# Kernel tuning notes

Measured on AMD Instinct MI355X. Metric: run time of the kernel, lower is better.

The kernel has to match this reference:

```python
import jax, jax.numpy as jnp
import numpy as np

L = 2048      # sequence length (self.len)
DIM = 1024    # model dim
DPOS = 128    # positional encoding dim
B = 4
EPS = 1e-5


def make_pe(length, d):
    # standard sinusoidal positional encoding, shape [length, d]
    pos = np.arange(length)[:, None].astype(np.float32)
    div = np.exp(-np.arange(0, d, 2).astype(np.float32) * (np.log(10000.0) / d))
    pe = np.zeros((length, d), dtype=np.float32)
    pe[:, 0::2] = np.sin(pos * div)
    pe[:, 1::2] = np.cos(pos * div)
    return jnp.asarray(pe)


def setup_inputs() -> dict:
    key = jax.random.key(0)
    ks = jax.random.split(key, 16)
    s = lambda fan_in: 1.0 / np.sqrt(fan_in)
    inp = {
        "z": jax.random.normal(ks[0], (B, L, DIM), jnp.float32),
        "x": jax.random.normal(ks[1], (B, L, DIM), jnp.float32),
        "a": jax.random.normal(ks[2], (1,), jnp.float32),
        "pe": make_pe(L, DPOS),
        # torch Linear weights stored [out, in]
        "w_pos1": jax.random.normal(ks[3], (DPOS + DIM, DPOS), jnp.float32) * s(DPOS),
        "b_pos1": jnp.zeros((DPOS + DIM,), jnp.float32),
        "w_pos2": jax.random.normal(ks[4], (DIM, DPOS + DIM), jnp.float32) * s(DPOS + DIM),
        "b_pos2": jnp.zeros((DIM,), jnp.float32),
        "w1": jax.random.normal(ks[5], (DIM * 2, DIM), jnp.float32) * s(DIM),
        "b1": jnp.zeros((DIM * 2,), jnp.float32),
        "w2": jax.random.normal(ks[6], (DIM, DIM * 2), jnp.float32) * s(DIM * 2),
        "b2": jnp.zeros((DIM,), jnp.float32),
        "w3": jax.random.normal(ks[7], (DIM * 2, DIM), jnp.float32) * s(DIM),
        "b3": jnp.zeros((DIM * 2,), jnp.float32),
        "w4": jax.random.normal(ks[8], (DIM, DIM * 2), jnp.float32) * s(DIM * 2),
        "b4": jnp.zeros((DIM,), jnp.float32),
        "ln_g": jnp.ones((DIM,), jnp.float32),
        "ln_b": jnp.zeros((DIM,), jnp.float32),
    }
    return inp


def _layer_norm(v, g, b):
    mu = jnp.mean(v, axis=-1, keepdims=True)
    var = jnp.var(v, axis=-1, keepdims=True)
    return (v - mu) * jax.lax.rsqrt(var + EPS) * g + b


def _lin(v, w, b):
    return v @ w.T + b


def reference(z, x, a, pe, w_pos1, b_pos1, w_pos2, b_pos2,
              w1, b1, w2, b2, w3, b3, w4, b4, ln_g, ln_b):
    zn = _layer_norm(z, ln_g, ln_b)                       # [B, L, D]
    fz = jnp.fft.rfft(zn, n=2 * L, axis=1)                # [B, L+1, D] complex
    expa = jnp.exp(a)                                     # [1]
    window = jnp.exp(-jnp.arange(L, dtype=jnp.float32) * expa)  # [L]
    h = _lin(pe, w_pos1, b_pos1)                          # [L, DPOS+D]
    h = jax.nn.gelu(h, approximate=False)
    h = _lin(h, w_pos2, b_pos2)                           # [L, D] (dropout eval = id)
    wfh = jnp.fft.rfft(window[:, None] * h, n=2 * L, axis=0)  # [L+1, D]
    cwhz = jnp.fft.irfft(wfh * fz, axis=1)[:, :L, :]      # [B, L, D]
    x1 = _lin(x, w1, b1)
    x1 = jax.nn.gelu(x1, approximate=False)
    x1 = _lin(x1, w2, b2)
    x1 = x1 * cwhz + z
    y = _layer_norm(x1, ln_g, ln_b)
    y = _lin(y, w3, b3)
    y = jax.nn.gelu(y, approximate=False)
    y = _lin(y, w4, b4)
    return y + x1
```

## Files before the change

### kernel.cpp

```cpp
#include <hip/hip_runtime.h>
#include <hip/hip_bf16.h>
#include <cmath>

typedef __hip_bfloat16 bf16;
typedef __attribute__((ext_vector_type(8))) short bf16x8;
typedef __attribute__((ext_vector_type(4))) float f32x4;

static __device__ __forceinline__ float b2f(bf16 v) { return __bfloat162float(v); }
static __device__ __forceinline__ bf16 f2b(float v) { return __float2bfloat16(v); }
static __device__ __forceinline__ float us2f(unsigned short u) {
  return __uint_as_float(((unsigned)u) << 16);
}

static __device__ __forceinline__ void gl2lds16(const bf16* g, bf16* l) {
  __builtin_amdgcn_global_load_lds(
      (const __attribute__((address_space(1))) void*)g,
      (__attribute__((address_space(3))) void*)l, 16, 0, 0);
}

static __device__ __forceinline__ float gelu_fast(float v) {
  float u = v * (0.7978845608f + 0.0356774081f * v * v);
  float e = __expf(2.f * u);
  return v * (e * __frcp_rn(e + 1.f));
}

struct CvtSegs { const float* src[7]; int blk_off[8]; };
__global__ __launch_bounds__(256) void cvt7_k(CvtSegs s, bf16* __restrict__ dst0)
{
  int b = blockIdx.x;
  int seg = 0;
#pragma unroll
  for (int i = 0; i < 6; ++i) seg += (b >= s.blk_off[i + 1]) ? 1 : 0;
  const float* src = s.src[seg] + (size_t)(b - s.blk_off[seg]) * 1024;
  bf16* dst = dst0 + (size_t)b * 1024;
  int idx = threadIdx.x * 4;
  float4 v = *(const float4*)(src + idx);
  union { bf16 bb[4]; ushort4 u; } o;
  o.bb[0] = f2b(v.x); o.bb[1] = f2b(v.y); o.bb[2] = f2b(v.z); o.bb[3] = f2b(v.w);
  *(ushort4*)(dst + idx) = o.u;
}

__global__ __launch_bounds__(256) void cvt_k(const float* __restrict__ in,
                                             bf16* __restrict__ out, int n)
{
  int idx = (blockIdx.x * 256 + threadIdx.x) * 4;
  if (idx >= n) return;
  float4 v = *(const float4*)(in + idx);
  union { bf16 b[4]; ushort4 u; } o;
  o.b[0] = f2b(v.x); o.b[1] = f2b(v.y); o.b[2] = f2b(v.z); o.b[3] = f2b(v.w);
  *(ushort4*)(out + idx) = o.u;
}

__global__ __launch_bounds__(256) void ln_k(const float* __restrict__ X, bf16* __restrict__ Y,
                                            const float* __restrict__ gamma,
                                            const float* __restrict__ beta)
{
  __shared__ float red[16];
  const int row = blockIdx.x, tid = threadIdx.x;
  float4 v = *(const float4*)(X + (size_t)row * 1024 + tid * 4);
  float s  = v.x + v.y + v.z + v.w;
  float s2 = v.x * v.x + v.y * v.y + v.z * v.z + v.w * v.w;
#pragma unroll
  for (int m = 32; m; m >>= 1) { s += __shfl_xor(s, m, 64); s2 += __shfl_xor(s2, m, 64); }
  const int wid = tid >> 6;
  if ((tid & 63) == 0) { red[wid] = s; red[wid + 8] = s2; }
  __syncthreads();
  s  = red[0] + red[1] + red[2] + red[3];
  s2 = red[8] + red[9] + red[10] + red[11];
  const float mu  = s * (1.f / 1024.f);
  const float var = s2 * (1.f / 1024.f) - mu * mu;
  const float rs  = rsqrtf(var + 1e-5f);
  float4 g = *(const float4*)(gamma + tid * 4);
  float4 bt = *(const float4*)(beta + tid * 4);
  union { bf16 b[4]; ushort4 u; } o;
  o.b[0] = f2b((v.x - mu) * rs * g.x + bt.x);
  o.b[1] = f2b((v.y - mu) * rs * g.y + bt.y);
  o.b[2] = f2b((v.z - mu) * rs * g.z + bt.z);
  o.b[3] = f2b((v.w - mu) * rs * g.w + bt.w);
  *(ushort4*)(Y + (size_t)row * 1024 + tid * 4) = o.u;
}

template<int EPI>
__global__ __launch_bounds__(256, 3) void gemm_k(
    const bf16* __restrict__ A, const bf16* __restrict__ W,
    const float* __restrict__ bias, void* __restrict__ Out,
    const void* __restrict__ aux0, const void* __restrict__ aux1,
    int M, int N, int K)
{
  __shared__ bf16 As[3][128 * 32];
  __shared__ bf16 Bs[3][128 * 32];
  const int tid = threadIdx.x;
  const int wid = tid >> 6, lane = tid & 63;
  const int quad = lane >> 4, l16 = lane & 15;
  const int wm = wid >> 1, wn = wid & 1;
  const int m0 = blockIdx.y * 128, n0 = blockIdx.x * 128;

  f32x4 acc[4][4];
#pragma unroll
  for (int i = 0; i < 4; ++i)
#pragma unroll
    for (int j = 0; j < 4; ++j) acc[i][j] = (f32x4){0.f, 0.f, 0.f, 0.f};

  const bf16 *ga[2], *gb[2];
  int ldso[2];
#pragma unroll
  for (int r = 0; r < 2; ++r) {
    int p = r * 256 + wid * 64 + lane;
    int row = p >> 2;
    int sko = ((p & 3) ^ ((p >> 3) & 3)) << 3;
    ga[r] = A + (size_t)(m0 + row) * K + sko;
    gb[r] = W + (size_t)(n0 + row) * K + sko;
    ldso[r] = (r * 256 + wid * 64) * 8;
  }
  int apos[4], bpos[4];
#pragma unroll
  for (int i = 0; i < 4; ++i) {
    int ar = wm * 64 + i * 16 + l16;
    apos[i] = (ar * 4 + (quad ^ ((ar >> 1) & 3))) * 8;
    int br = wn * 64 + i * 16 + l16;
    bpos[i] = (br * 4 + (quad ^ ((br >> 1) & 3))) * 8;
  }

  const int niter = K >> 5;
#pragma unroll
  for (int t = 0; t < 2; ++t)
#pragma unroll
    for (int r = 0; r < 2; ++r) {
      gl2lds16(ga[r] + t * 32, &As[t][ldso[r]]);
      gl2lds16(gb[r] + t * 32, &Bs[t][ldso[r]]);
    }

  int cur = 0;
  for (int k = 0; k < niter; ++k) {
    if (k == niter - 1) { asm volatile("s_waitcnt vmcnt(0)" ::: "memory"); }
    else               { asm volatile("s_waitcnt vmcnt(4)" ::: "memory"); }
    asm volatile("s_barrier" ::: "memory");

    const bf16* as = As[cur];
    const bf16* bs = Bs[cur];
    bf16x8 af[4], bfr[4];
#pragma unroll
    for (int i = 0; i < 4; ++i) af[i]  = *(const bf16x8*)(as + apos[i]);
#pragma unroll
    for (int j = 0; j < 4; ++j) bfr[j] = *(const bf16x8*)(bs + bpos[j]);
    asm volatile("s_waitcnt lgkmcnt(0)" ::: "memory");

    if (k + 2 < niter) {
      int nb = cur + 2; if (nb >= 3) nb -= 3;
#pragma unroll
      for (int r = 0; r < 2; ++r) {
        gl2lds16(ga[r] + (k + 2) * 32, &As[nb][ldso[r]]);
        gl2lds16(gb[r] + (k + 2) * 32, &Bs[nb][ldso[r]]);
      }
    }
#pragma unroll
    for (int i = 0; i < 4; ++i)
#pragma unroll
      for (int j = 0; j < 4; ++j)
        acc[i][j] = __builtin_amdgcn_mfma_f32_16x16x32_bf16(af[i], bfr[j], acc[i][j], 0, 0, 0);
    cur += 1; if (cur == 3) cur = 0;
  }

  float expa = 0.f;
  if (EPI == 1) expa = expf(((const float*)aux0)[0]);
#pragma unroll
  for (int i = 0; i < 4; ++i) {
    const int gm_base = m0 + wm * 64 + i * 16 + quad * 4;
#pragma unroll
    for (int j = 0; j < 4; ++j) {
      const int gn = n0 + wn * 64 + j * 16 + l16;
      const float bv = bias[gn];
#pragma unroll
      for (int r = 0; r < 4; ++r) {
        const int gm = gm_base + r;
        const size_t off = (size_t)gm * N + gn;
        float v = acc[i][j][r] + bv;
        if (EPI == 0) ((bf16*)Out)[off] = f2b(gelu_fast(v));
        else if (EPI == 1) ((float*)Out)[off] = v * expf(-(float)gm * expa);
        else if (EPI == 2) ((float*)Out)[off] = v * ((const float*)aux0)[off] + ((const float*)aux1)[off];
        else ((float*)Out)[off] = v + ((const float*)aux0)[off];
      }
    }
  }
}

template<int EPI>
__global__ __launch_bounds__(256, 2) void gemm256_k(
    const bf16* __restrict__ A, const bf16* __restrict__ W,
    const float* __restrict__ bias, void* __restrict__ Out,
    const void* __restrict__ aux0, const void* __restrict__ aux1,
    int M, int N, int K)
{
  __shared__ bf16 As[3][128 * 32];
  __shared__ bf16 Bs[3][256 * 32];
  const int tid = threadIdx.x;
  const int wid = tid >> 6, lane = tid & 63;
  const int quad = lane >> 4, l16 = lane & 15;
  const int wm = wid >> 1, wn = wid & 1;
  const int m0 = blockIdx.y * 128, n0 = blockIdx.x * 256;

  f32x4 acc[4][8];
#pragma unroll
  for (int i = 0; i < 4; ++i)
#pragma unroll
    for (int j = 0; j < 8; ++j) acc[i][j] = (f32x4){0.f, 0.f, 0.f, 0.f};

  const bf16 *ga[2], *gb[4];
  int ldsoA[2], ldsoB[4];
#pragma unroll
  for (int r = 0; r < 2; ++r) {
    int p = r * 256 + tid;
    int row = p >> 2;
    int sko = ((p & 3) ^ ((p >> 3) & 3)) << 3;
    ga[r] = A + (size_t)(m0 + row) * K + sko;
    ldsoA[r] = (r * 256 + wid * 64) * 8;
  }
#pragma unroll
  for (int r = 0; r < 4; ++r) {
    int p = r * 256 + tid;
    int row = p >> 2;
    int sko = ((p & 3) ^ ((p >> 3) & 3)) << 3;
    gb[r] = W + (size_t)(n0 + row) * K + sko;
    ldsoB[r] = (r * 256 + wid * 64) * 8;
  }
  int apos[4], bpos[8];
#pragma unroll
  for (int i = 0; i < 4; ++i) {
    int ar = wm * 64 + i * 16 + l16;
    apos[i] = (ar * 4 + (quad ^ ((ar >> 1) & 3))) * 8;
  }
#pragma unroll
  for (int j = 0; j < 8; ++j) {
    int br = wn * 128 + j * 16 + l16;
    bpos[j] = (br * 4 + (quad ^ ((br >> 1) & 3))) * 8;
  }

  const int niter = K >> 5;
#pragma unroll
  for (int t = 0; t < 2; ++t) {
#pragma unroll
    for (int r = 0; r < 2; ++r) gl2lds16(ga[r] + t * 32, &As[t][ldsoA[r]]);
#pragma unroll
    for (int r = 0; r < 4; ++r) gl2lds16(gb[r] + t * 32, &Bs[t][ldsoB[r]]);
  }

  int cur = 0;
  for (int k = 0; k < niter; ++k) {
    if (k == niter - 1) { asm volatile("s_waitcnt vmcnt(0)" ::: "memory"); }
    else               { asm volatile("s_waitcnt vmcnt(6)" ::: "memory"); }
    asm volatile("s_barrier" ::: "memory");

    const bf16* as = As[cur];
    const bf16* bs = Bs[cur];
    bf16x8 af[4], bfr[8];
#pragma unroll
    for (int i = 0; i < 4; ++i) af[i]  = *(const bf16x8*)(as + apos[i]);
#pragma unroll
    for (int j = 0; j < 8; ++j) bfr[j] = *(const bf16x8*)(bs + bpos[j]);
    asm volatile("s_waitcnt lgkmcnt(0)" ::: "memory");

    if (k + 2 < niter) {
      int nb = cur + 2; if (nb >= 3) nb -= 3;
#pragma unroll
      for (int r = 0; r < 2; ++r) gl2lds16(ga[r] + (k + 2) * 32, &As[nb][ldsoA[r]]);
#pragma unroll
      for (int r = 0; r < 4; ++r) gl2lds16(gb[r] + (k + 2) * 32, &Bs[nb][ldsoB[r]]);
    }
#pragma unroll
    for (int i = 0; i < 4; ++i)
#pragma unroll
      for (int j = 0; j < 8; ++j)
        acc[i][j] = __builtin_amdgcn_mfma_f32_16x16x32_bf16(af[i], bfr[j], acc[i][j], 0, 0, 0);
    cur += 1; if (cur == 3) cur = 0;
  }

#pragma unroll
  for (int i = 0; i < 4; ++i) {
    const int gm_base = m0 + wm * 64 + i * 16 + quad * 4;
#pragma unroll
    for (int j = 0; j < 8; ++j) {
      const int gn = n0 + wn * 128 + j * 16 + l16;
      const float bv = bias[gn];
#pragma unroll
      for (int r = 0; r < 4; ++r) {
        const int gm = gm_base + r;
        const size_t off = (size_t)gm * N + gn;
        float v = acc[i][j][r] + bv;
        if (EPI == 0) ((bf16*)Out)[off] = f2b(gelu_fast(v));
        else if (EPI == 2) ((float*)Out)[off] = v * ((const float*)aux0)[off] + ((const float*)aux1)[off];
        else ((float*)Out)[off] = v + ((const float*)aux0)[off];
      }
    }
  }
}

__global__ __launch_bounds__(256) void conv_k(
    const bf16* __restrict__ zn,
    const float* __restrict__ wh,
    const float* __restrict__ a,
    float* __restrict__ out)
{
  __shared__ float whs[64 * 64];
  __shared__ float znt[128 * 64];
  const int tid = threadIdx.x;
  const int dd = tid & 63, ttg = tid >> 6;
  const int t0 = blockIdx.x * 64, d0 = blockIdx.y * 64, b = blockIdx.z;
  const float expa = expf(a[0]);
  const float smax = 20.7f / expa;
  const unsigned short* znu = (const unsigned short*)zn;

  float acc[16];
#pragma unroll
  for (int q = 0; q < 16; ++q) acc[q] = 0.f;

  for (int sb = 0; sb <= t0 + 63; sb += 64) {
    if ((float)sb > smax) break;
    float4 wv4[4];
#pragma unroll
    for (int i = 0; i < 4; ++i) {
      int cc = tid + 256 * i;
      int row = cc >> 4, dq = (cc & 15) * 4;
      wv4[i] = *(const float4*)&wh[(size_t)(sb + row) * 1024 + d0 + dq];
    }
    ushort4 zv4[8];
#pragma unroll
    for (int i = 0; i < 8; ++i) {
      int cc = tid + 256 * i;
      int row = cc >> 4, dq = (cc & 15) * 4;
      int u = t0 - sb - 64 + row;
      zv4[i] = (u >= 0) ? *(const ushort4*)&znu[((size_t)b * 2048 + u) * 1024 + d0 + dq]
                        : make_ushort4(0, 0, 0, 0);
    }
#pragma unroll
    for (int i = 0; i < 4; ++i) {
      int cc = tid + 256 * i;
      *(float4*)&whs[(cc >> 4) * 64 + (cc & 15) * 4] = wv4[i];
    }
#pragma unroll
    for (int i = 0; i < 8; ++i) {
      int cc = tid + 256 * i;
      float4 o;
      o.x = us2f(zv4[i].x); o.y = us2f(zv4[i].y); o.z = us2f(zv4[i].z); o.w = us2f(zv4[i].w);
      *(float4*)&znt[(cc >> 4) * 64 + (cc & 15) * 4] = o;
    }
    __syncthreads();

    float win[16];
#pragma unroll
    for (int q = 0; q < 16; ++q) win[q] = znt[(ttg * 16 + q + 64) * 64 + dd];
#pragma unroll
    for (int ss = 0; ss < 64; ++ss) {
      float wv = whs[ss * 64 + dd];
#pragma unroll
      for (int q = 0; q < 16; ++q) acc[q] += wv * win[q];
      if (ss < 63) {
#pragma unroll
        for (int q = 15; q >= 1; --q) win[q] = win[q - 1];
        win[0] = znt[(ttg * 16 + 63 - ss) * 64 + dd];
      }
    }
    __syncthreads();
  }
#pragma unroll
  for (int q = 0; q < 16; ++q) {
    int t = t0 + ttg * 16 + q;
    out[((size_t)b * 2048 + t) * 1024 + d0 + dd] = acc[q];
  }
}

extern "C" void kernel_launch(void* const* d_in, const int* in_sizes, int n_in,
                              void* d_out, int out_size, void* d_ws, size_t ws_size,
                              hipStream_t stream)
{
  const float* z      = (const float*)d_in[0];
  const float* x      = (const float*)d_in[1];
  const float* a      = (const float*)d_in[2];
  const float* pe     = (const float*)d_in[3];
  const float* w_pos1 = (const float*)d_in[4];
  const float* b_pos1 = (const float*)d_in[5];
  const float* w_pos2 = (const float*)d_in[6];
  const float* b_pos2 = (const float*)d_in[7];
  const float* w1     = (const float*)d_in[8];
  const float* b1     = (const float*)d_in[9];
  const float* w2     = (const float*)d_in[10];
  const float* b2     = (const float*)d_in[11];
  const float* w3     = (const float*)d_in[12];
  const float* b3     = (const float*)d_in[13];
  const float* w4     = (const float*)d_in[14];
  const float* b4     = (const float*)d_in[15];
  const float* ln_g   = (const float*)d_in[16];
  const float* ln_b   = (const float*)d_in[17];

  char* ws = (char*)d_ws;
  bf16* pe_bf  = (bf16*)(ws + 0);
  bf16* wp1_bf = (bf16*)(ws + 524288);
  bf16* wp2_bf = (bf16*)(ws + 819200);
  bf16* w1_bf  = (bf16*)(ws + 3178496);
  bf16* w2_bf  = (bf16*)(ws + 7372800);
  bf16* w3_bf  = (bf16*)(ws + 11567104);
  bf16* w4_bf  = (bf16*)(ws + 15761408);
  bf16* h1     = (bf16*)(ws + 19955712);
  bf16* zn_bf  = (bf16*)(ws + 24674304);
  bf16* x_bf   = (bf16*)(ws + 41451520);
  float* wh    = (float*)(ws + 58228736);
  float* cwhz  = (float*)(ws + 66617344);
  bf16*  x1n   = (bf16*)(ws + 66617344);
  bf16*  g     = (bf16*)(ws + 100171776);
  float* x1    = (float*)(ws + 24674304);
  float* out   = (float*)d_out;

  CvtSegs segs;
  segs.src[0] = pe;  segs.src[1] = w_pos1; segs.src[2] = w_pos2;
  segs.src[3] = w1;  segs.src[4] = w2;     segs.src[5] = w3; segs.src[6] = w4;
  int bo[8] = {0, 256, 400, 1552, 3600, 5648, 7696, 9744};
  for (int i = 0; i < 8; ++i) segs.blk_off[i] = bo[i];
  cvt7_k<<<9744, 256, 0, stream>>>(segs, (bf16*)ws);
  cvt_k<<<8192, 256, 0, stream>>>(x, x_bf, 8388608);

  ln_k<<<8192, 256, 0, stream>>>(z, zn_bf, ln_g, ln_b);
  gemm_k<0><<<dim3(9, 16), 256, 0, stream>>>(pe_bf, wp1_bf, b_pos1, h1, nullptr, nullptr, 2048, 1152, 128);
  gemm_k<1><<<dim3(8, 16), 256, 0, stream>>>(h1, wp2_bf, b_pos2, wh, a, nullptr, 2048, 1024, 1152);
  conv_k<<<dim3(32, 16, 4), 256, 0, stream>>>(zn_bf, wh, a, cwhz);
  gemm256_k<0><<<dim3(8, 64), 256, 0, stream>>>(x_bf, w1_bf, b1, g, nullptr, nullptr, 8192, 2048, 1024);
  gemm_k<2><<<dim3(8, 64), 256, 0, stream>>>(g, w2_bf, b2, x1, cwhz, z, 8192, 1024, 2048);
  ln_k<<<8192, 256, 0, stream>>>(x1, x1n, ln_g, ln_b);
  gemm256_k<0><<<dim3(8, 64), 256, 0, stream>>>(x1n, w3_bf, b3, g, nullptr, nullptr, 8192, 2048, 1024);
  gemm_k<3><<<dim3(8, 64), 256, 0, stream>>>(g, w4_bf, b4, out, x1, nullptr, 8192, 1024, 2048);
}
```

Baseline: 432.5 us.

## Remap GEMM workgroups per XCD and drop 128x256 GEMM variant

Adds a block-index remap in the 128x128 GEMM so consecutive tiles land on the same XCD, improving L2 locality across the chiplets. Removes the 128x256-tile GEMM and runs the two up-projection GEMMs with the 128x128 kernel on a doubled grid. This trades the larger tile's operand reuse for more workgroups and better cache locality from the swizzle.

```diff
diff --git a/kernel.cpp b/kernel.cpp
--- a/kernel.cpp
+++ b/kernel.cpp
@@ -93,7 +93,17 @@
   const int wid = tid >> 6, lane = tid & 63;
   const int quad = lane >> 4, l16 = lane & 15;
   const int wm = wid >> 1, wn = wid & 1;
-  const int m0 = blockIdx.y * 128, n0 = blockIdx.x * 128;
+
+  const int nwg = gridDim.x * gridDim.y;
+  int lid = blockIdx.y * gridDim.x + blockIdx.x;
+  {
+    const int q = nwg >> 3, r = nwg & 7;
+    const int xcd = lid & 7, loc = lid >> 3;
+    const int base = (xcd < r) ? xcd * (q + 1) : r * (q + 1) + (xcd - r) * q;
+    lid = base + loc;
+  }
+  const int bx = lid % gridDim.x, by = lid / gridDim.x;
+  const int m0 = by * 128, n0 = bx * 128;
 
   f32x4 acc[4][4];
 #pragma unroll
@@ -177,116 +187,6 @@
         float v = acc[i][j][r] + bv;
         if (EPI == 0) ((bf16*)Out)[off] = f2b(gelu_fast(v));
         else if (EPI == 1) ((float*)Out)[off] = v * expf(-(float)gm * expa);
-        else if (EPI == 2) ((float*)Out)[off] = v * ((const float*)aux0)[off] + ((const float*)aux1)[off];
-        else ((float*)Out)[off] = v + ((const float*)aux0)[off];
-      }
-    }
-  }
-}
-
-template<int EPI>
-__global__ __launch_bounds__(256, 2) void gemm256_k(
-    const bf16* __restrict__ A, const bf16* __restrict__ W,
-    const float* __restrict__ bias, void* __restrict__ Out,
-    const void* __restrict__ aux0, const void* __restrict__ aux1,
-    int M, int N, int K)
-{
-  __shared__ bf16 As[3][128 * 32];
-  __shared__ bf16 Bs[3][256 * 32];
-  const int tid = threadIdx.x;
-  const int wid = tid >> 6, lane = tid & 63;
-  const int quad = lane >> 4, l16 = lane & 15;
-  const int wm = wid >> 1, wn = wid & 1;
-  const int m0 = blockIdx.y * 128, n0 = blockIdx.x * 256;
-
-  f32x4 acc[4][8];
-#pragma unroll
-  for (int i = 0; i < 4; ++i)
-#pragma unroll
-    for (int j = 0; j < 8; ++j) acc[i][j] = (f32x4){0.f, 0.f, 0.f, 0.f};
-
-  const bf16 *ga[2], *gb[4];
-  int ldsoA[2], ldsoB[4];
-#pragma unroll
-  for (int r = 0; r < 2; ++r) {
-    int p = r * 256 + tid;
-    int row = p >> 2;
-    int sko = ((p & 3) ^ ((p >> 3) & 3)) << 3;
-    ga[r] = A + (size_t)(m0 + row) * K + sko;
-    ldsoA[r] = (r * 256 + wid * 64) * 8;
-  }
-#pragma unroll
-  for (int r = 0; r < 4; ++r) {
-    int p = r * 256 + tid;
-    int row = p >> 2;
-    int sko = ((p & 3) ^ ((p >> 3) & 3)) << 3;
-    gb[r] = W + (size_t)(n0 + row) * K + sko;
-    ldsoB[r] = (r * 256 + wid * 64) * 8;
-  }
-  int apos[4], bpos[8];
-#pragma unroll
-  for (int i = 0; i < 4; ++i) {
-    int ar = wm * 64 + i * 16 + l16;
-    apos[i] = (ar * 4 + (quad ^ ((ar >> 1) & 3))) * 8;
-  }
-#pragma unroll
-  for (int j = 0; j < 8; ++j) {
-    int br = wn * 128 + j * 16 + l16;
-    bpos[j] = (br * 4 + (quad ^ ((br >> 1) & 3))) * 8;
-  }
-
-  const int niter = K >> 5;
-#pragma unroll
-  for (int t = 0; t < 2; ++t) {
-#pragma unroll
-    for (int r = 0; r < 2; ++r) gl2lds16(ga[r] + t * 32, &As[t][ldsoA[r]]);
-#pragma unroll
-    for (int r = 0; r < 4; ++r) gl2lds16(gb[r] + t * 32, &Bs[t][ldsoB[r]]);
-  }
-
-  int cur = 0;
-  for (int k = 0; k < niter; ++k) {
-    if (k == niter - 1) { asm volatile("s_waitcnt vmcnt(0)" ::: "memory"); }
-    else               { asm volatile("s_waitcnt vmcnt(6)" ::: "memory"); }
-    asm volatile("s_barrier" ::: "memory");
-
-    const bf16* as = As[cur];
-    const bf16* bs = Bs[cur];
-    bf16x8 af[4], bfr[8];
-#pragma unroll
-    for (int i = 0; i < 4; ++i) af[i]  = *(const bf16x8*)(as + apos[i]);
-#pragma unroll
-    for (int j = 0; j < 8; ++j) bfr[j] = *(const bf16x8*)(bs + bpos[j]);
-    asm volatile("s_waitcnt lgkmcnt(0)" ::: "memory");
-
-    if (k + 2 < niter) {
-      int nb = cur + 2; if (nb >= 3) nb -= 3;
-#pragma unroll
-      for (int r = 0; r < 2; ++r) gl2lds16(ga[r] + (k + 2) * 32, &As[nb][ldsoA[r]]);
-#pragma unroll
-      for (int r = 0; r < 4; ++r) gl2lds16(gb[r] + (k + 2) * 32, &Bs[nb][ldsoB[r]]);
-    }
-#pragma unroll
-    for (int i = 0; i < 4; ++i)
-#pragma unroll
-      for (int j = 0; j < 8; ++j)
-        acc[i][j] = __builtin_amdgcn_mfma_f32_16x16x32_bf16(af[i], bfr[j], acc[i][j], 0, 0, 0);
-    cur += 1; if (cur == 3) cur = 0;
-  }
-
-#pragma unroll
-  for (int i = 0; i < 4; ++i) {
-    const int gm_base = m0 + wm * 64 + i * 16 + quad * 4;
-#pragma unroll
-    for (int j = 0; j < 8; ++j) {
-      const int gn = n0 + wn * 128 + j * 16 + l16;
-      const float bv = bias[gn];
-#pragma unroll
-      for (int r = 0; r < 4; ++r) {
-        const int gm = gm_base + r;
-        const size_t off = (size_t)gm * N + gn;
-        float v = acc[i][j][r] + bv;
-        if (EPI == 0) ((bf16*)Out)[off] = f2b(gelu_fast(v));
         else if (EPI == 2) ((float*)Out)[off] = v * ((const float*)aux0)[off] + ((const float*)aux1)[off];
         else ((float*)Out)[off] = v + ((const float*)aux0)[off];
       }
@@ -421,9 +321,9 @@
   gemm_k<0><<<dim3(9, 16), 256, 0, stream>>>(pe_bf, wp1_bf, b_pos1, h1, nullptr, nullptr, 2048, 1152, 128);
   gemm_k<1><<<dim3(8, 16), 256, 0, stream>>>(h1, wp2_bf, b_pos2, wh, a, nullptr, 2048, 1024, 1152);
   conv_k<<<dim3(32, 16, 4), 256, 0, stream>>>(zn_bf, wh, a, cwhz);
-  gemm256_k<0><<<dim3(8, 64), 256, 0, stream>>>(x_bf, w1_bf, b1, g, nullptr, nullptr, 8192, 2048, 1024);
+  gemm_k<0><<<dim3(16, 64), 256, 0, stream>>>(x_bf, w1_bf, b1, g, nullptr, nullptr, 8192, 2048, 1024);
   gemm_k<2><<<dim3(8, 64), 256, 0, stream>>>(g, w2_bf, b2, x1, cwhz, z, 8192, 1024, 2048);
   ln_k<<<8192, 256, 0, stream>>>(x1, x1n, ln_g, ln_b);
-  gemm256_k<0><<<dim3(8, 64), 256, 0, stream>>>(x1n, w3_bf, b3, g, nullptr, nullptr, 8192, 2048, 1024);
+  gemm_k<0><<<dim3(16, 64), 256, 0, stream>>>(x1n, w3_bf, b3, g, nullptr, nullptr, 8192, 2048, 1024);
   gemm_k<3><<<dim3(8, 64), 256, 0, stream>>>(g, w4_bf, b4, out, x1, nullptr, 8192, 1024, 2048);
 }
```

Measured after the change: 418.3 us. -3.3%, faster.

## Retile GEMMs to smaller output tiles and add XCD-aware workgroup swizzle

Applied to the files above, without the earlier changes.

Replaces the 128x256 GEMM kernel with a 128x64 tile variant (higher occupancy, launch bound 4) used for the N=1024 GEMMs. The 2048-wide GEMMs now use the 128x128 kernel. Both kernels remap block IDs so consecutive tiles land on the same XCD for L2 reuse. Smaller tiles raise the block count and occupancy on MI355X's many CUs, but lower per-block arithmetic intensity and add more A re-reads.

```diff
diff --git a/kernel.cpp b/kernel.cpp
--- a/kernel.cpp
+++ b/kernel.cpp
@@ -22,6 +22,13 @@
   float u = v * (0.7978845608f + 0.0356774081f * v * v);
   float e = __expf(2.f * u);
   return v * (e * __frcp_rn(e + 1.f));
+}
+
+static __device__ __forceinline__ int xcd_swz(int lid, int nwg) {
+  const int q = nwg >> 3, r = nwg & 7;
+  const int xcd = lid & 7, loc = lid >> 3;
+  const int base = (xcd < r) ? xcd * (q + 1) : r * (q + 1) + (xcd - r) * q;
+  return base + loc;
 }
 
 struct CvtSegs { const float* src[7]; int blk_off[8]; };
@@ -93,7 +100,11 @@
   const int wid = tid >> 6, lane = tid & 63;
   const int quad = lane >> 4, l16 = lane & 15;
   const int wm = wid >> 1, wn = wid & 1;
-  const int m0 = blockIdx.y * 128, n0 = blockIdx.x * 128;
+
+  const int nwg = gridDim.x * gridDim.y;
+  int lid = xcd_swz(blockIdx.y * gridDim.x + blockIdx.x, nwg);
+  const int bx = lid % gridDim.x, by = lid / gridDim.x;
+  const int m0 = by * 128, n0 = bx * 128;
 
   f32x4 acc[4][4];
 #pragma unroll
@@ -185,53 +196,57 @@
 }
 
 template<int EPI>
-__global__ __launch_bounds__(256, 2) void gemm256_k(
+__global__ __launch_bounds__(256, 4) void gemm64_k(
     const bf16* __restrict__ A, const bf16* __restrict__ W,
     const float* __restrict__ bias, void* __restrict__ Out,
     const void* __restrict__ aux0, const void* __restrict__ aux1,
     int M, int N, int K)
 {
   __shared__ bf16 As[3][128 * 32];
-  __shared__ bf16 Bs[3][256 * 32];
+  __shared__ bf16 Bs[3][64 * 32];
   const int tid = threadIdx.x;
   const int wid = tid >> 6, lane = tid & 63;
   const int quad = lane >> 4, l16 = lane & 15;
   const int wm = wid >> 1, wn = wid & 1;
-  const int m0 = blockIdx.y * 128, n0 = blockIdx.x * 256;
-
-  f32x4 acc[4][8];
+
+  const int nwg = gridDim.x * gridDim.y;
+  int lid = xcd_swz(blockIdx.y * gridDim.x + blockIdx.x, nwg);
+  const int bx = lid % gridDim.x, by = lid / gridDim.x;
+  const int m0 = by * 128, n0 = bx * 64;
+
+  f32x4 acc[4][2];
 #pragma unroll
   for (int i = 0; i < 4; ++i)
 #pragma unroll
-    for (int j = 0; j < 8; ++j) acc[i][j] = (f32x4){0.f, 0.f, 0.f, 0.f};
-
-  const bf16 *ga[2], *gb[4];
-  int ldsoA[2], ldsoB[4];
+    for (int j = 0; j < 2; ++j) acc[i][j] = (f32x4){0.f, 0.f, 0.f, 0.f};
+
+  const bf16 *ga[2], *gbp;
+  int ldsoA[2];
 #pragma unroll
   for (int r = 0; r < 2; ++r) {
-    int p = r * 256 + tid;
+    int p = r * 256 + wid * 64 + lane;
     int row = p >> 2;
     int sko = ((p & 3) ^ ((p >> 3) & 3)) << 3;
     ga[r] = A + (size_t)(m0 + row) * K + sko;
     ldsoA[r] = (r * 256 + wid * 64) * 8;
   }
-#pragma unroll
-  for (int r = 0; r < 4; ++r) {
-    int p = r * 256 + tid;
+  {
+    int p = wid * 64 + lane;
     int row = p >> 2;
     int sko = ((p & 3) ^ ((p >> 3) & 3)) << 3;
-    gb[r] = W + (size_t)(n0 + row) * K + sko;
-    ldsoB[r] = (r * 256 + wid * 64) * 8;
-  }
-  int apos[4], bpos[8];
+    gbp = W + (size_t)(n0 + row) * K + sko;
+  }
+  const int ldsoB = wid * 64 * 8;
+
+  int apos[4], bpos[2];
 #pragma unroll
   for (int i = 0; i < 4; ++i) {
     int ar = wm * 64 + i * 16 + l16;
     apos[i] = (ar * 4 + (quad ^ ((ar >> 1) & 3))) * 8;
   }
 #pragma unroll
-  for (int j = 0; j < 8; ++j) {
-    int br = wn * 128 + j * 16 + l16;
+  for (int j = 0; j < 2; ++j) {
+    int br = wn * 32 + j * 16 + l16;
     bpos[j] = (br * 4 + (quad ^ ((br >> 1) & 3))) * 8;
   }
 
@@ -240,46 +255,46 @@
   for (int t = 0; t < 2; ++t) {
 #pragma unroll
     for (int r = 0; r < 2; ++r) gl2lds16(ga[r] + t * 32, &As[t][ldsoA[r]]);
-#pragma unroll
-    for (int r = 0; r < 4; ++r) gl2lds16(gb[r] + t * 32, &Bs[t][ldsoB[r]]);
+    gl2lds16(gbp + t * 32, &Bs[t][ldsoB]);
   }
 
   int cur = 0;
   for (int k = 0; k < niter; ++k) {
     if (k == niter - 1) { asm volatile("s_waitcnt vmcnt(0)" ::: "memory"); }
-    else               { asm volatile("s_waitcnt vmcnt(6)" ::: "memory"); }
+    else               { asm volatile("s_waitcnt vmcnt(3)" ::: "memory"); }
     asm volatile("s_barrier" ::: "memory");
 
     const bf16* as = As[cur];
     const bf16* bs = Bs[cur];
-    bf16x8 af[4], bfr[8];
+    bf16x8 af[4], bfr[2];
 #pragma unroll
     for (int i = 0; i < 4; ++i) af[i]  = *(const bf16x8*)(as + apos[i]);
 #pragma unroll
-    for (int j = 0; j < 8; ++j) bfr[j] = *(const bf16x8*)(bs + bpos[j]);
+    for (int j = 0; j < 2; ++j) bfr[j] = *(const bf16x8*)(bs + bpos[j]);
     asm volatile("s_waitcnt lgkmcnt(0)" ::: "memory");
 
     if (k + 2 < niter) {
       int nb = cur + 2; if (nb >= 3) nb -= 3;
 #pragma unroll
       for (int r = 0; r < 2; ++r) gl2lds16(ga[r] + (k + 2) * 32, &As[nb][ldsoA[r]]);
-#pragma unroll
-      for (int r = 0; r < 4; ++r) gl2lds16(gb[r] + (k + 2) * 32, &Bs[nb][ldsoB[r]]);
+      gl2lds16(gbp + (k + 2) * 32, &Bs[nb][ldsoB]);
     }
 #pragma unroll
     for (int i = 0; i < 4; ++i)
 #pragma unroll
-      for (int j = 0; j < 8; ++j)
+      for (int j = 0; j < 2; ++j)
         acc[i][j] = __builtin_amdgcn_mfma_f32_16x16x32_bf16(af[i], bfr[j], acc[i][j], 0, 0, 0);
     cur += 1; if (cur == 3) cur = 0;
   }
 
+  float expa = 0.f;
+  if (EPI == 1) expa = expf(((const float*)aux0)[0]);
 #pragma unroll
   for (int i = 0; i < 4; ++i) {
     const int gm_base = m0 + wm * 64 + i * 16 + quad * 4;
 #pragma unroll
-    for (int j = 0; j < 8; ++j) {
-      const int gn = n0 + wn * 128 + j * 16 + l16;
+    for (int j = 0; j < 2; ++j) {
+      const int gn = n0 + wn * 32 + j * 16 + l16;
       const float bv = bias[gn];
 #pragma unroll
       for (int r = 0; r < 4; ++r) {
@@ -287,6 +302,7 @@
         const size_t off = (size_t)gm * N + gn;
         float v = acc[i][j][r] + bv;
         if (EPI == 0) ((bf16*)Out)[off] = f2b(gelu_fast(v));
+        else if (EPI == 1) ((float*)Out)[off] = v * expf(-(float)gm * expa);
         else if (EPI == 2) ((float*)Out)[off] = v * ((const float*)aux0)[off] + ((const float*)aux1)[off];
         else ((float*)Out)[off] = v + ((const float*)aux0)[off];
       }
@@ -419,11 +435,11 @@
 
   ln_k<<<8192, 256, 0, stream>>>(z, zn_bf, ln_g, ln_b);
   gemm_k<0><<<dim3(9, 16), 256, 0, stream>>>(pe_bf, wp1_bf, b_pos1, h1, nullptr, nullptr, 2048, 1152, 128);
-  gemm_k<1><<<dim3(8, 16), 256, 0, stream>>>(h1, wp2_bf, b_pos2, wh, a, nullptr, 2048, 1024, 1152);
+  gemm64_k<1><<<dim3(16, 16), 256, 0, stream>>>(h1, wp2_bf, b_pos2, wh, a, nullptr, 2048, 1024, 1152);
   conv_k<<<dim3(32, 16, 4), 256, 0, stream>>>(zn_bf, wh, a, cwhz);
-  gemm256_k<0><<<dim3(8, 64), 256, 0, stream>>>(x_bf, w1_bf, b1, g, nullptr, nullptr, 8192, 2048, 1024);
-  gemm_k<2><<<dim3(8, 64), 256, 0, stream>>>(g, w2_bf, b2, x1, cwhz, z, 8192, 1024, 2048);
+  gemm_k<0><<<dim3(16, 64), 256, 0, stream>>>(x_bf, w1_bf, b1, g, nullptr, nullptr, 8192, 2048, 1024);
+  gemm64_k<2><<<dim3(16, 64), 256, 0, stream>>>(g, w2_bf, b2, x1, cwhz, z, 8192, 1024, 2048);
   ln_k<<<8192, 256, 0, stream>>>(x1, x1n, ln_g, ln_b);
-  gemm256_k<0><<<dim3(8, 64), 256, 0, stream>>>(x1n, w3_bf, b3, g, nullptr, nullptr, 8192, 2048, 1024);
-  gemm_k<3><<<dim3(8, 64), 256, 0, stream>>>(g, w4_bf, b4, out, x1, nullptr, 8192, 1024, 2048);
-}
+  gemm_k<0><<<dim3(16, 64), 256, 0, stream>>>(x1n, w3_bf, b3, g, nullptr, nullptr, 8192, 2048, 1024);
+  gemm64_k<3><<<dim3(16, 64), 256, 0, stream>>>(g, w4_bf, b4, out, x1, nullptr, 8192, 1024, 2048);
+}
```

New measurement: 444.3 us. 2.7% more time.
